# Kernel tuning notes

Hardware: AMD Instinct MI355X
Metric: run time of the kernel (lower is better)

Reference implementation:

```python
import jax, jax.numpy as jnp
import numpy as np

B, S, E = 2, 2048, 2048
HQ, HKV, D = 16, 4, 128
WINDOW = 512
ROPE_BASE = 10000.0


def apply_rope(x):
    # x: [B, H, S, D]; rotate-half RoPE, positions start at 0 (prefill, no cache)
    half = x.shape[-1] // 2
    inv_freq = 1.0 / (ROPE_BASE ** (jnp.arange(half, dtype=jnp.float32) / half))
    ang = jnp.arange(x.shape[2], dtype=jnp.float32)[:, None] * inv_freq[None, :]  # [S, half]
    cos, sin = jnp.cos(ang), jnp.sin(ang)
    x1, x2 = x[..., :half], x[..., half:]
    return jnp.concatenate([x1 * cos - x2 * sin, x1 * sin + x2 * cos], axis=-1)


def setup_inputs() -> dict:
    key = jax.random.key(0)
    ks = jax.random.split(key, 9)
    sc = 0.02
    return {
        "x": jax.random.normal(ks[0], (B, S, E), dtype=jnp.float32),
        "Wq": jax.random.normal(ks[1], (HQ * D, E), dtype=jnp.float32) * sc,
        "bq": jnp.zeros((HQ * D,), dtype=jnp.float32),
        "Wk": jax.random.normal(ks[2], (HKV * D, E), dtype=jnp.float32) * sc,
        "bk": jnp.zeros((HKV * D,), dtype=jnp.float32),
        "Wv": jax.random.normal(ks[3], (HKV * D, E), dtype=jnp.float32) * sc,
        "bv": jnp.zeros((HKV * D,), dtype=jnp.float32),
        "Wo": jax.random.normal(ks[4], (E, HQ * D), dtype=jnp.float32) * sc,
        "bo": jnp.zeros((E,), dtype=jnp.float32),
    }


def reference(x, Wq, bq, Wk, bk, Wv, bv, Wo, bo):
    b, s, _ = x.shape
    group = HQ // HKV
    # projections (torch Linear: y = x @ W.T + b)
    Q = (x @ Wq.T + bq).reshape(b, s, HQ, D).transpose(0, 2, 1, 3)     # [B,HQ,S,D]
    K = (x @ Wk.T + bk).reshape(b, s, HKV, D).transpose(0, 2, 1, 3)    # [B,HKV,S,D]
    V = (x @ Wv.T + bv).reshape(b, s, HKV, D).transpose(0, 2, 1, 3)
    Q = apply_rope(Q)
    K = apply_rope(K)
    # GQA: group query heads per KV head instead of repeating K/V (same math)
    Qg = Q.reshape(b, HKV, group, s, D)
    scores = jnp.einsum('bkgqd,bkyd->bkgqy', Qg, K) / jnp.sqrt(jnp.float32(D))
    # sliding-window causal mask: j <= i and i - j <= window_size
    i = jnp.arange(s)[:, None]
    j = jnp.arange(s)[None, :]
    allowed = (j <= i) & ((i - j) <= WINDOW)
    scores = jnp.where(allowed, scores, jnp.float32(-jnp.inf))
    w = jax.nn.softmax(scores, axis=-1)
    out = jnp.einsum('bkgqy,bkyd->bkgqd', w, V)                        # [B,HKV,G,S,D]
    out = out.reshape(b, HQ, s, D).transpose(0, 2, 1, 3).reshape(b, s, HQ * D)
    out = out @ Wo.T + bo  # dropout is identity at inference
    return out
```

## Files before the change

### kernel.cpp

```cpp
#include <hip/hip_runtime.h>
#include <hip/hip_bf16.h>

typedef unsigned short u16;
typedef unsigned int u32;
typedef __attribute__((ext_vector_type(4))) unsigned short ushort4_t;
typedef __attribute__((ext_vector_type(8))) short short8;
typedef __attribute__((ext_vector_type(4))) float f32x4;

#define B_ 2
#define S_ 2048
#define E_ 2048
#define HQ_ 16
#define HKV_ 4
#define D_ 128
#define WINDOW_ 512

static __device__ __forceinline__ float bf2f(u16 u) {
    union { unsigned int i; float f; } v; v.i = ((unsigned int)u) << 16; return v.f;
}
static __device__ __forceinline__ u16 f2bf(float f) {
    unsigned int x = __float_as_uint(f);
    unsigned int r = (x + 0x7fffu + ((x >> 16) & 1u)) >> 16;
    return (u16)r;
}

static __device__ __forceinline__ void gload_lds16(const u16* g, u16* l) {
    __builtin_amdgcn_global_load_lds(
        (const __attribute__((address_space(1))) unsigned int*)g,
        (__attribute__((address_space(3))) unsigned int*)l,
        16, 0, 0);
}

static __device__ __forceinline__ int detect_fp32(const u16* wq, int* cnt_sh) {
    if (threadIdx.x == 0) *cnt_sh = 0;
    __syncthreads();
    int c = 0;
    #pragma unroll
    for (int k = 0; k < 4; ++k) {
        u16 v = wq[threadIdx.x * 4 + k];
        if (((v >> 7) & 0xFF) >= 0x90) c++;
    }
    atomicAdd(cnt_sh, c);
    __syncthreads();
    return (*cnt_sh >= 64) ? 1 : 0;
}

#define C_WQ   8388608u
#define C_WK   12582912u
#define C_WV   13631488u
#define C_BQ   14680064u
#define C_BK   14682112u
#define C_BV   14682624u
#define C_WO   14683136u
#define C_BO   18877440u
#define NTOT   18879488u

__global__ __launch_bounds__(256) void convert_kernel(
    const void* p0, const void* p1, const void* p2, const void* p3, const void* p4,
    const void* p5, const void* p6, const void* p7, const void* p8,
    u16* __restrict__ C, int* __restrict__ flagout)
{
    __shared__ int cnt;
    const int f = detect_fp32((const u16*)p1, &cnt);
    if (blockIdx.x == 0 && threadIdx.x == 0) *flagout = f;

    unsigned int idx = (blockIdx.x * 256u + threadIdx.x) * 4u;
    if (idx >= NTOT) return;

    const void* src; unsigned int local;
    if      (idx < C_WQ) { src = p0; local = idx; }
    else if (idx < C_WK) { src = p1; local = idx - C_WQ; }
    else if (idx < C_WV) { src = p3; local = idx - C_WK; }
    else if (idx < C_BQ) { src = p5; local = idx - C_WV; }
    else if (idx < C_BK) { src = p2; local = idx - C_BQ; }
    else if (idx < C_BV) { src = p4; local = idx - C_BK; }
    else if (idx < C_WO) { src = p6; local = idx - C_BV; }
    else if (idx < C_BO) { src = p7; local = idx - C_WO; }
    else                 { src = p8; local = idx - C_BO; }

    ushort4_t o;
    if (f) {
        float4 v = *(const float4*)((const float*)src + local);
        o[0] = f2bf(v.x); o[1] = f2bf(v.y); o[2] = f2bf(v.z); o[3] = f2bf(v.w);
    } else {
        o = *(const ushort4_t*)((const u16*)src + local);
    }
    *(ushort4_t*)(C + idx) = o;
}

#define TBK 32

__global__ __launch_bounds__(256) void gemm128(
    const u16* __restrict__ A, const u16* __restrict__ W,
    const u16* __restrict__ bias, u16* __restrict__ C,
    int M, int N, int K)
{
    __shared__ __align__(16) u16 As[128 * TBK];
    __shared__ __align__(16) u16 Bs[128 * TBK];

    const int m0 = blockIdx.y * 128, n0 = blockIdx.x * 128;

    const int t = threadIdx.x;
    const int wv = t >> 6, lane = t & 63;
    const int waveM = wv >> 1, waveN = wv & 1;
    const int quad = lane >> 4, l16 = lane & 15;

    const int lrow = lane >> 2;
    const int lcol = (lane & 3) * 8;

    f32x4 acc[4][4];
    #pragma unroll
    for (int mi = 0; mi < 4; ++mi)
        #pragma unroll
        for (int ni = 0; ni < 4; ++ni)
            acc[mi][ni] = (f32x4){0.f, 0.f, 0.f, 0.f};

    const u16* ga = A + (size_t)(m0 + wv * 32 + lrow) * K + lcol;
    const u16* gb = W + (size_t)(n0 + wv * 32 + lrow) * K + lcol;
    u16* la0 = As + (wv * 32) * TBK;
    u16* la1 = As + (wv * 32 + 16) * TBK;
    u16* lb0 = Bs + (wv * 32) * TBK;
    u16* lb1 = Bs + (wv * 32 + 16) * TBK;

    for (int k0 = 0; k0 < K; k0 += TBK) {
        __syncthreads();
        gload_lds16(ga + k0, la0);
        gload_lds16(ga + k0 + (size_t)16 * K, la1);
        gload_lds16(gb + k0, lb0);
        gload_lds16(gb + k0 + (size_t)16 * K, lb1);
        __syncthreads();

        short8 af[4];
        #pragma unroll
        for (int mi = 0; mi < 4; ++mi)
            af[mi] = *(const short8*)(As + (waveM * 64 + mi * 16 + l16) * TBK + quad * 8);
        #pragma unroll
        for (int ni = 0; ni < 4; ++ni) {
            short8 bf = *(const short8*)(Bs + (waveN * 64 + ni * 16 + l16) * TBK + quad * 8);
            #pragma unroll
            for (int mi = 0; mi < 4; ++mi)
                acc[mi][ni] = __builtin_amdgcn_mfma_f32_16x16x32_bf16(af[mi], bf, acc[mi][ni], 0, 0, 0);
        }
    }

    #pragma unroll
    for (int mi = 0; mi < 4; ++mi) {
        #pragma unroll
        for (int ni = 0; ni < 4; ++ni) {
            int row0 = m0 + waveM * 64 + mi * 16 + quad * 4;
            int col  = n0 + waveN * 64 + ni * 16 + l16;
            float bb = bf2f(bias[col]);
            #pragma unroll
            for (int r = 0; r < 4; ++r)
                C[(size_t)(row0 + r) * N + col] = f2bf(acc[mi][ni][r] + bb);
        }
    }
}

__global__ __launch_bounds__(256) void gemm128_out(
    const u16* __restrict__ A, const u16* __restrict__ W,
    const u16* __restrict__ bias, void* __restrict__ Cout,
    int M, int N, int K, const int* __restrict__ flagp)
{
    __shared__ __align__(16) u16 As[128 * TBK];
    __shared__ __align__(16) u16 Bs[128 * TBK];

    const int m0 = blockIdx.y * 128, n0 = blockIdx.x * 128;

    const int t = threadIdx.x;
    const int wv = t >> 6, lane = t & 63;
    const int waveM = wv >> 1, waveN = wv & 1;
    const int quad = lane >> 4, l16 = lane & 15;

    const int lrow = lane >> 2;
    const int lcol = (lane & 3) * 8;

    f32x4 acc[4][4];
    #pragma unroll
    for (int mi = 0; mi < 4; ++mi)
        #pragma unroll
        for (int ni = 0; ni < 4; ++ni)
            acc[mi][ni] = (f32x4){0.f, 0.f, 0.f, 0.f};

    const u16* ga = A + (size_t)(m0 + wv * 32 + lrow) * K + lcol;
    const u16* gb = W + (size_t)(n0 + wv * 32 + lrow) * K + lcol;
    u16* la0 = As + (wv * 32) * TBK;
    u16* la1 = As + (wv * 32 + 16) * TBK;
    u16* lb0 = Bs + (wv * 32) * TBK;
    u16* lb1 = Bs + (wv * 32 + 16) * TBK;

    for (int k0 = 0; k0 < K; k0 += TBK) {
        __syncthreads();
        gload_lds16(ga + k0, la0);
        gload_lds16(ga + k0 + (size_t)16 * K, la1);
        gload_lds16(gb + k0, lb0);
        gload_lds16(gb + k0 + (size_t)16 * K, lb1);
        __syncthreads();

        short8 af[4];
        #pragma unroll
        for (int mi = 0; mi < 4; ++mi)
            af[mi] = *(const short8*)(As + (waveM * 64 + mi * 16 + l16) * TBK + quad * 8);
        #pragma unroll
        for (int ni = 0; ni < 4; ++ni) {
            short8 bf = *(const short8*)(Bs + (waveN * 64 + ni * 16 + l16) * TBK + quad * 8);
            #pragma unroll
            for (int mi = 0; mi < 4; ++mi)
                acc[mi][ni] = __builtin_amdgcn_mfma_f32_16x16x32_bf16(af[mi], bf, acc[mi][ni], 0, 0, 0);
        }
    }

    const int f = *flagp;
    #pragma unroll
    for (int mi = 0; mi < 4; ++mi) {
        #pragma unroll
        for (int ni = 0; ni < 4; ++ni) {
            int row0 = m0 + waveM * 64 + mi * 16 + quad * 4;
            int col  = n0 + waveN * 64 + ni * 16 + l16;
            float bb = bf2f(bias[col]);
            #pragma unroll
            for (int r = 0; r < 4; ++r) {
                float val = acc[mi][ni][r] + bb;
                size_t idx = (size_t)(row0 + r) * N + col;
                if (f) ((float*)Cout)[idx] = val;
                else   ((u16*)Cout)[idx]   = f2bf(val);
            }
        }
    }
}

#define ROPE_BLOCKS 20480

__global__ __launch_bounds__(256) void rope_transpose(
    u16* __restrict__ QKV, u16* __restrict__ VT)
{
    if (blockIdx.x < ROPE_BLOCKS) {
        const size_t qtot = (size_t)B_ * S_ * HQ_ * 64;
        size_t idx = (size_t)blockIdx.x * 256 + threadIdx.x;

        int d; size_t tok; u16* p;
        if (idx < qtot) {
            d = (int)(idx & 63);
            size_t th = idx >> 6;
            int h = (int)(th & 15);
            tok = th >> 4;
            p = QKV + tok * 3072 + h * 128 + d;
        } else {
            size_t r = idx - qtot;
            d = (int)(r & 63);
            size_t th = r >> 6;
            int kh = (int)(th & 3);
            tok = th >> 2;
            p = QKV + tok * 3072 + 2048 + kh * 128 + d;
        }
        int s = (int)(tok & (S_ - 1));

        float x1 = bf2f(p[0]);
        float x2 = bf2f(p[64]);
        float inv_freq = __expf(-0.14391156514f * (float)d);
        float ang = (float)s * inv_freq;
        float sn, cs;
        __sincosf(ang, &sn, &cs);
        p[0]  = f2bf(x1 * cs - x2 * sn);
        p[64] = f2bf(x1 * sn + x2 * cs);
    } else {
        const int bid = blockIdx.x - ROPE_BLOCKS;
        const int t = threadIdx.x;
        const int s_blk = bid & 63;
        const int dh = (bid >> 6) & 1;
        const int bkh = bid >> 7;
        const int b = bkh >> 2, kh = bkh & 3;

        const int d = dh * 64 + (t & 63);
        const int s0 = s_blk * 32 + (t >> 6) * 8;

        const u16* src = QKV + (size_t)(b * S_ + s0) * 3072 + 2560 + kh * 128 + d;
        short8 v;
        #pragma unroll
        for (int j = 0; j < 8; ++j)
            v[j] = (short)src[(size_t)j * 3072];
        *(short8*)(VT + ((size_t)(bkh * 128 + d)) * S_ + s0) = v;
    }
}

__global__ __launch_bounds__(256) void attn_mfma(
    const u16* __restrict__ QKV, const u16* __restrict__ VT, u16* __restrict__ O)
{
    __shared__ __align__(16) u16 Ks[32 * 136];
    __shared__ __align__(16) u16 Vs[128 * 40];
    __shared__ __align__(16) u16 ps[4][16 * 40];

    const int t = threadIdx.x;
    const int wv = t >> 6, lane = t & 63;
    const int quad = lane >> 4, l16 = lane & 15;

    const int h = blockIdx.x & 15;
    const int tile = (blockIdx.x >> 4) & 31;
    const int b = blockIdx.x >> 9;
    const int kh = h >> 2;

    const int i0b = tile * 64;
    const int i0w = i0b + wv * 16;
    const float scale = 0.08838834764831845f;
    const float CEXP = 8.0f;

    short8 qf[4];
    {
        const u16* qrow = QKV + (size_t)(b * S_ + i0w + l16) * 3072 + h * 128 + quad * 8;
        #pragma unroll
        for (int kc = 0; kc < 4; ++kc)
            qf[kc] = *(const short8*)(qrow + kc * 32);
    }

    short8 ones;
    #pragma unroll
    for (int j = 0; j < 8; ++j) ones[j] = (short)0x3F80;

    f32x4 oc[8];
    #pragma unroll
    for (int c = 0; c < 8; ++c) oc[c] = (f32x4){0.f, 0.f, 0.f, 0.f};
    f32x4 ocl = (f32x4){0.f, 0.f, 0.f, 0.f};

    int jlo = i0b - WINDOW_; if (jlo < 0) jlo = 0;
    const int nblk = (i0b + 64 - jlo) >> 5;

    const u16* VTb = VT + (size_t)(b * 4 + kh) * 128 * S_;

    for (int blk = 0; blk < nblk; ++blk) {
        const int jbase = jlo + blk * 32;
        __syncthreads();
        #pragma unroll
        for (int it = 0; it < 2; ++it) {
            int idx = it * 256 + t;
            int key = idx >> 4;
            int c8  = (idx & 15) * 8;
            int row = ((key & 1) << 4) | (key >> 1);
            short8 kvv = *(const short8*)(QKV + (size_t)(b * S_ + jbase + key) * 3072 + 2048 + kh * 128 + c8);
            *(short8*)(Ks + row * 136 + c8) = kvv;
        }
        #pragma unroll
        for (int it = 0; it < 2; ++it) {
            int idx = it * 256 + t;
            int d = idx >> 2;
            int q4 = idx & 3;
            short8 vvv = *(const short8*)(VTb + (size_t)d * S_ + jbase + q4 * 8);
            *(short8*)(Vs + d * 40 + q4 * 8) = vvv;
        }
        __syncthreads();

        bool active = (jbase <= i0w + 15) && (jbase + 31 >= i0w - WINDOW_);
        if (!active) continue;

        f32x4 sc0 = {0.f,0.f,0.f,0.f}, sc1 = {0.f,0.f,0.f,0.f};
        #pragma unroll
        for (int kc = 0; kc < 4; ++kc) {
            short8 kb0 = *(const short8*)(Ks + l16 * 136 + kc * 32 + quad * 8);
            short8 kb1 = *(const short8*)(Ks + (16 + l16) * 136 + kc * 32 + quad * 8);
            sc0 = __builtin_amdgcn_mfma_f32_16x16x32_bf16(qf[kc], kb0, sc0, 0, 0, 0);
            sc1 = __builtin_amdgcn_mfma_f32_16x16x32_bf16(qf[kc], kb1, sc1, 0, 0, 0);
        }

        const int j0 = jbase + 2 * l16;
        const int iq = i0w + quad * 4;
        u16* pw = ps[wv];
        #pragma unroll
        for (int r = 0; r < 4; ++r) {
            int i = iq + r;
            bool ok0 = (unsigned)(i - j0)     <= (unsigned)WINDOW_;
            bool ok1 = (unsigned)(i - j0 - 1) <= (unsigned)WINDOW_;
            float p0 = ok0 ? __expf(sc0[r] * scale - CEXP) : 0.f;
            float p1 = ok1 ? __expf(sc1[r] * scale - CEXP) : 0.f;
            u32 pk = ((u32)f2bf(p1) << 16) | (u32)f2bf(p0);
            *(u32*)(pw + (quad * 4 + r) * 40 + 2 * l16) = pk;
        }
        short8 pa = *(const short8*)(pw + l16 * 40 + quad * 8);

        #pragma unroll
        for (int c = 0; c < 8; ++c) {
            short8 vb = *(const short8*)(Vs + (c * 16 + l16) * 40 + quad * 8);
            oc[c] = __builtin_amdgcn_mfma_f32_16x16x32_bf16(pa, vb, oc[c], 0, 0, 0);
        }
        ocl = __builtin_amdgcn_mfma_f32_16x16x32_bf16(pa, ones, ocl, 0, 0, 0);
    }

    float inv0[4];
    #pragma unroll
    for (int r = 0; r < 4; ++r) inv0[r] = 1.0f / ocl[r];
    #pragma unroll
    for (int c = 0; c < 8; ++c) {
        #pragma unroll
        for (int r = 0; r < 4; ++r) {
            O[((size_t)(b * S_ + i0w + quad * 4 + r) * HQ_ + h) * D_ + c * 16 + l16] =
                f2bf(oc[c][r] * inv0[r]);
        }
    }
}

extern "C" void kernel_launch(void* const* d_in, const int* in_sizes, int n_in,
                              void* d_out, int out_size, void* d_ws, size_t ws_size,
                              hipStream_t stream)
{
    char* ws = (char*)d_ws;
    u16* Cc   = (u16*)ws;
    int* flag = (int*)(ws + 37758976);
    u16* QKV  = (u16*)(ws + 37759232);
    u16* Ab   = (u16*)(ws + 37759232 + 25165824);

    const u16* xb    = Cc;
    u16*       VT    = Cc;
    const u16* Wqkv  = Cc + C_WQ;
    const u16* bqkv  = Cc + C_BQ;
    const u16* Wob   = Cc + C_WO;
    const u16* bob   = Cc + C_BO;

    const int M = B_ * S_;
    dim3 blk(256);

    convert_kernel<<<dim3(NTOT / 4 / 256), blk, 0, stream>>>(
        d_in[0], d_in[1], d_in[2], d_in[3], d_in[4], d_in[5], d_in[6], d_in[7], d_in[8],
        Cc, flag);

    gemm128<<<dim3(3072 / 128, M / 128), blk, 0, stream>>>(xb, Wqkv, bqkv, QKV, M, 3072, E_);

    rope_transpose<<<dim3(ROPE_BLOCKS + 1024), blk, 0, stream>>>(QKV, VT);

    attn_mfma<<<dim3(B_ * HQ_ * (S_ / 64)), blk, 0, stream>>>(QKV, VT, Ab);

    gemm128_out<<<dim3(E_ / 128, M / 128), blk, 0, stream>>>(Ab, Wob, bob, d_out, M, E_, HQ_ * D_, flag);
}
```

Baseline: 325.7 us.

## Replace QKV projection GEMM with 256x256 double-buffered swizzled LDS pipeline

Swaps the 128x128-tile QKV GEMM, which synchronized twice per 32-wide K step, for a 512-thread 256x256-tile kernel with a K step of 64. Global-to-LDS loads are double-buffered and interleaved across four compute phases, using explicit vmcnt waits, XOR-swizzled LDS addressing to avoid bank conflicts, and setprio around the MFMA bursts. The aim is to raise arithmetic intensity and hide load latency. The cost is 128 KB of LDS per block and only 12x16=192 blocks, which may underfill the GPU's compute units.

New measurement: 329.7 us. No clear change (+1.2%).

```diff
diff --git a/kernel.cpp b/kernel.cpp
--- a/kernel.cpp
+++ b/kernel.cpp
@@ -88,74 +88,135 @@
     *(ushort4_t*)(C + idx) = o;
 }
 
-#define TBK 32
-
-__global__ __launch_bounds__(256) void gemm128(
+__global__ __launch_bounds__(512, 2) void gemm256(
     const u16* __restrict__ A, const u16* __restrict__ W,
     const u16* __restrict__ bias, u16* __restrict__ C,
     int M, int N, int K)
 {
-    __shared__ __align__(16) u16 As[128 * TBK];
-    __shared__ __align__(16) u16 Bs[128 * TBK];
-
-    const int m0 = blockIdx.y * 128, n0 = blockIdx.x * 128;
-
+    __shared__ __align__(16) u16 lds[65536];
+
+    const int m0 = blockIdx.y * 256, n0 = blockIdx.x * 256;
     const int t = threadIdx.x;
     const int wv = t >> 6, lane = t & 63;
-    const int waveM = wv >> 1, waveN = wv & 1;
+    const int wm = wv >> 2, wn = wv & 3;
     const int quad = lane >> 4, l16 = lane & 15;
-
-    const int lrow = lane >> 2;
-    const int lcol = (lane & 3) * 8;
-
-    f32x4 acc[4][4];
-    #pragma unroll
-    for (int mi = 0; mi < 4; ++mi)
+    const int h3 = l16 & 7;
+
+    const int rr = t >> 3;
+    const int sblk = ((t & 7) ^ (rr & 7)) * 8;
+
+    const u16* Asrc = A + (size_t)(m0 + rr) * K + sblk;
+    const u16* Bsrc = W + (size_t)(n0 + rr) * K + sblk;
+    u16* ldsA = lds + wv * 512;
+    u16* ldsB = lds + 16384 + wv * 512;
+
+#define STAGE_A(slot, Qi, k0) gload_lds16(Asrc + (size_t)((Qi) * 64) * K + (k0), ldsA + (slot) * 32768 + (Qi) * 4096)
+#define STAGE_B(slot, Qi, k0) gload_lds16(Bsrc + (size_t)((Qi) * 64) * K + (k0), ldsB + (slot) * 32768 + (Qi) * 4096)
+
+    f32x4 acc[8][4];
+    #pragma unroll
+    for (int mi = 0; mi < 8; ++mi)
         #pragma unroll
         for (int ni = 0; ni < 4; ++ni)
             acc[mi][ni] = (f32x4){0.f, 0.f, 0.f, 0.f};
 
-    const u16* ga = A + (size_t)(m0 + wv * 32 + lrow) * K + lcol;
-    const u16* gb = W + (size_t)(n0 + wv * 32 + lrow) * K + lcol;
-    u16* la0 = As + (wv * 32) * TBK;
-    u16* la1 = As + (wv * 32 + 16) * TBK;
-    u16* lb0 = Bs + (wv * 32) * TBK;
-    u16* lb1 = Bs + (wv * 32 + 16) * TBK;
-
-    for (int k0 = 0; k0 < K; k0 += TBK) {
-        __syncthreads();
-        gload_lds16(ga + k0, la0);
-        gload_lds16(ga + k0 + (size_t)16 * K, la1);
-        gload_lds16(gb + k0, lb0);
-        gload_lds16(gb + k0 + (size_t)16 * K, lb1);
-        __syncthreads();
-
-        short8 af[4];
-        #pragma unroll
-        for (int mi = 0; mi < 4; ++mi)
-            af[mi] = *(const short8*)(As + (waveM * 64 + mi * 16 + l16) * TBK + quad * 8);
+    const int NT = K / 64;
+
+    #pragma unroll
+    for (int q = 0; q < 4; ++q) STAGE_A(0, q, 0);
+    #pragma unroll
+    for (int q = 0; q < 4; ++q) STAGE_B(0, q, 0);
+    __builtin_amdgcn_sched_barrier(0);
+    #pragma unroll
+    for (int q = 0; q < 4; ++q) STAGE_A(1, q, 64);
+    #pragma unroll
+    for (int q = 0; q < 4; ++q) STAGE_B(1, q, 64);
+    __builtin_amdgcn_sched_barrier(0);
+
+    for (int kt = 0; kt < NT; ++kt) {
+        const int slot = kt & 1;
+        const u16* As = lds + slot * 32768;
+        const u16* Bs = As + 16384;
+
+        if (kt == 0)           asm volatile("s_waitcnt vmcnt(8)" ::: "memory");
+        else if (kt == NT - 1) asm volatile("s_waitcnt vmcnt(0)" ::: "memory");
+        else                   asm volatile("s_waitcnt vmcnt(2)" ::: "memory");
+        __builtin_amdgcn_s_barrier();
+        __builtin_amdgcn_sched_barrier(0);
+
+        const int kB = (kt + 1) * 64;
+        const int kA = (kt + 2) * 64;
+        const int sB = slot ^ 1;
+        const bool doB = (kt >= 1) && (kt <= NT - 2);
+        const bool doA = (kt <= NT - 3);
+
+        #pragma unroll
+        for (int ph = 0; ph < 4; ++ph) {
+            const int qm = ph >> 1, qn = ph & 1;
+
+            short8 af[4][2], bfr[2][2];
+            #pragma unroll
+            for (int f = 0; f < 4; ++f) {
+                const int r = wm * 128 + qm * 64 + f * 16 + l16;
+                #pragma unroll
+                for (int kk = 0; kk < 2; ++kk)
+                    af[f][kk] = *(const short8*)(As + r * 64 + (((kk * 4 + quad) ^ h3) << 3));
+            }
+            #pragma unroll
+            for (int g = 0; g < 2; ++g) {
+                const int r = wn * 64 + qn * 32 + g * 16 + l16;
+                #pragma unroll
+                for (int kk = 0; kk < 2; ++kk)
+                    bfr[g][kk] = *(const short8*)(Bs + r * 64 + (((kk * 4 + quad) ^ h3) << 3));
+            }
+
+            if (ph == 0 && doB) { STAGE_A(sB, 1, kB); STAGE_A(sB, 3, kB);
+                                  STAGE_B(sB, 0, kB); STAGE_B(sB, 1, kB); }
+            if (ph == 1 && doB) { STAGE_B(sB, 2, kB); STAGE_B(sB, 3, kB); }
+            if (ph == 2 && doA) { STAGE_A(slot, 0, kA); }
+            if (ph == 3 && doA) { STAGE_A(slot, 2, kA); }
+
+            __builtin_amdgcn_sched_barrier(0);
+            __builtin_amdgcn_s_barrier();
+            asm volatile("s_waitcnt lgkmcnt(0)" ::: "memory");
+            __builtin_amdgcn_sched_barrier(0);
+
+            __builtin_amdgcn_s_setprio(1);
+            #pragma unroll
+            for (int g = 0; g < 2; ++g)
+                #pragma unroll
+                for (int f = 0; f < 4; ++f)
+                    #pragma unroll
+                    for (int kk = 0; kk < 2; ++kk)
+                        acc[qm * 4 + f][qn * 2 + g] =
+                            __builtin_amdgcn_mfma_f32_16x16x32_bf16(
+                                af[f][kk], bfr[g][kk], acc[qm * 4 + f][qn * 2 + g], 0, 0, 0);
+            __builtin_amdgcn_s_setprio(0);
+
+            __builtin_amdgcn_sched_barrier(0);
+            __builtin_amdgcn_s_barrier();
+            __builtin_amdgcn_sched_barrier(0);
+        }
+    }
+
+#undef STAGE_A
+#undef STAGE_B
+
+    #pragma unroll
+    for (int mi = 0; mi < 8; ++mi) {
         #pragma unroll
         for (int ni = 0; ni < 4; ++ni) {
-            short8 bf = *(const short8*)(Bs + (waveN * 64 + ni * 16 + l16) * TBK + quad * 8);
-            #pragma unroll
-            for (int mi = 0; mi < 4; ++mi)
-                acc[mi][ni] = __builtin_amdgcn_mfma_f32_16x16x32_bf16(af[mi], bf, acc[mi][ni], 0, 0, 0);
-        }
-    }
-
-    #pragma unroll
-    for (int mi = 0; mi < 4; ++mi) {
-        #pragma unroll
-        for (int ni = 0; ni < 4; ++ni) {
-            int row0 = m0 + waveM * 64 + mi * 16 + quad * 4;
-            int col  = n0 + waveN * 64 + ni * 16 + l16;
-            float bb = bf2f(bias[col]);
+            const int row0 = m0 + wm * 128 + mi * 16 + quad * 4;
+            const int col  = n0 + wn * 64 + ni * 16 + l16;
+            const float bb = bf2f(bias[col]);
             #pragma unroll
             for (int r = 0; r < 4; ++r)
                 C[(size_t)(row0 + r) * N + col] = f2bf(acc[mi][ni][r] + bb);
         }
     }
 }
+
+#define TBK 32
 
 __global__ __launch_bounds__(256) void gemm128_out(
     const u16* __restrict__ A, const u16* __restrict__ W,
@@ -420,7 +481,8 @@
         d_in[0], d_in[1], d_in[2], d_in[3], d_in[4], d_in[5], d_in[6], d_in[7], d_in[8],
         Cc, flag);
 
-    gemm128<<<dim3(3072 / 128, M / 128), blk, 0, stream>>>(xb, Wqkv, bqkv, QKV, M, 3072, E_);
+    gemm256<<<dim3(3072 / 256, M / 256), dim3(512), 0, stream>>>(
+        xb, Wqkv, bqkv, QKV, M, 3072, E_);
 
     rope_transpose<<<dim3(ROPE_BLOCKS + 1024), blk, 0, stream>>>(QKV, VT);
 
```
